# Kernel tuning notes

Hardware: AMD Instinct MI355X
Metric: run time of the kernel (lower is better)

## Reference

```python
import jax, jax.numpy as jnp
import numpy as np

HID = 128

def setup_inputs() -> dict:
    key = jax.random.key(0)
    ks = jax.random.split(key, 16)
    T, N, E = 32, 10000, 160000
    features = jax.random.normal(ks[0], (T, N, 1), dtype=jnp.float32)
    src = jax.random.randint(ks[1], (E,), 0, N)
    dst = jax.random.randint(ks[2], (E,), 0, N)
    s = 0.1
    # GraphConv params (stored as [in,out] so y = x @ W + b)
    W1 = jax.random.normal(ks[3], (1, 32), dtype=jnp.float32) * s
    b1 = jnp.zeros((32,), jnp.float32)
    W2 = jax.random.normal(ks[4], (32, HID), dtype=jnp.float32) * s
    b2 = jnp.zeros((HID,), jnp.float32)
    # attention-pool gate nn.Linear(128,1)
    gate_w = jax.random.normal(ks[5], (HID, 1), dtype=jnp.float32) * s
    gate_b = jnp.zeros((1,), jnp.float32)
    # GRU params, PyTorch layout: [3H, in], gate order (r, z, n)
    W_ih = jax.random.normal(ks[6], (3 * HID, HID), dtype=jnp.float32) * s
    W_hh = jax.random.normal(ks[7], (3 * HID, HID), dtype=jnp.float32) * s
    b_ih = jnp.zeros((3 * HID,), jnp.float32)
    b_hh = jnp.zeros((3 * HID,), jnp.float32)
    # dense layers ([in,out])
    d1_w = jax.random.normal(ks[8], (HID, 16), dtype=jnp.float32) * s
    d1_b = jnp.zeros((16,), jnp.float32)
    d2_w = jax.random.normal(ks[9], (16, 4), dtype=jnp.float32) * s
    d2_b = jnp.zeros((4,), jnp.float32)
    return {"features": features, "src": src, "dst": dst,
            "W1": W1, "b1": b1, "W2": W2, "b2": b2,
            "gate_w": gate_w, "gate_b": gate_b,
            "W_ih": W_ih, "W_hh": W_hh, "b_ih": b_ih, "b_hh": b_hh,
            "d1_w": d1_w, "d1_b": d1_b, "d2_w": d2_w, "d2_b": d2_b}


def reference(features, src, dst, W1, b1, W2, b2, gate_w, gate_b,
              W_ih, W_hh, b_ih, b_hh, d1_w, d1_b, d2_w, d2_b):
    T, N, _ = features.shape
    E = src.shape[0]
    ones = jnp.ones((E,), features.dtype)
    out_deg = jnp.clip(jax.ops.segment_sum(ones, src, num_segments=N), 1.0)
    in_deg = jnp.clip(jax.ops.segment_sum(ones, dst, num_segments=N), 1.0)
    norm_out = out_deg ** -0.5  # DGL GraphConv norm='both' (src side)
    norm_in = in_deg ** -0.5    # dst side

    def gconv(h, W, b):
        # h: [N, F] -> scale by src norm, gather, scatter-add to dst, scale, linear, SiLU
        msg = (h * norm_out[:, None])[src]               # [E, F]
        agg = jax.ops.segment_sum(msg, dst, num_segments=N)  # [N, F]
        return jax.nn.silu((agg * norm_in[:, None]) @ W + b)

    def per_frame(f):  # f: [N,1]
        return gconv(gconv(f, W1, b1), W2, b2)  # [N, HID]

    h = jax.vmap(per_frame)(features)  # [T, N, HID]

    # GlobalAttentionPooling: softmax over nodes of gate_nn(h)
    gate = h @ gate_w + gate_b                 # [T, N, 1]
    alpha = jax.nn.softmax(gate, axis=1)
    pooled = jnp.sum(alpha * h, axis=1)        # [T, HID]

    # single-layer GRU, batch=1, take final hidden state
    def gru_step(hprev, x):
        gi = x @ W_ih.T + b_ih
        gh = hprev @ W_hh.T + b_hh
        i_r, i_z, i_n = jnp.split(gi, 3)
        h_r, h_z, h_n = jnp.split(gh, 3)
        r = jax.nn.sigmoid(i_r + h_r)
        z = jax.nn.sigmoid(i_z + h_z)
        n = jnp.tanh(i_n + r * h_n)
        hnew = (1.0 - z) * n + z * hprev
        return hnew, None

    h0 = jnp.zeros((HID,), features.dtype)
    hT, _ = jax.lax.scan(gru_step, h0, pooled)

    out = jax.nn.silu(hT @ d1_w + d1_b)
    out = jax.nn.silu(out @ d2_w + d2_b)
    return jax.nn.sigmoid(out).reshape(1, 4)
```

## Files before the change

kernel.cpp:

```cpp
#include <hip/hip_runtime.h>
#include <stdint.h>

#define T_FRAMES 32
#define NNODES 10000
#define NEDGES 160000
#define HID 128
#define GXL 157

#define H1_SCALE 512.0f
#define H1_INV   (1.0f/512.0f)

typedef short v8s __attribute__((ext_vector_type(8)));
typedef float v4f __attribute__((ext_vector_type(4)));

static __device__ __forceinline__ ushort f2bf(float f){
  uint32_t u = __float_as_uint(f);
  u += 0x7FFFu + ((u >> 16) & 1u);
  return (ushort)(u >> 16);
}
static __device__ __forceinline__ float fsigm(float x){
  return __fdividef(1.0f, 1.0f + __expf(-x));
}
static __device__ __forceinline__ float fsilu(float x){
  return x * fsigm(x);
}
static __device__ __forceinline__ float ftanh(float x){
  return 2.0f * fsigm(2.0f * x) - 1.0f;
}


__global__ void k_degree(const int* __restrict__ src, const int* __restrict__ dst,
                         int* cnt_out, int* cnt_in, int E){
  int e = blockIdx.x*blockDim.x + threadIdx.x;
  if (e < E){
    atomicAdd(&cnt_out[src[e]], 1);
    atomicAdd(&cnt_in[dst[e]], 1);
  }
}

__global__ void __launch_bounds__(1024) k_scan(const int* __restrict__ cnt_in,
                                               const int* __restrict__ cnt_out,
                                               int* row_ptr, int* cursor,
                                               float* norm_out, float* norm_in, int N){
  __shared__ int wsum[16];
  __shared__ int carry_s, total_s;
  int tid = threadIdx.x;
  int lane = tid & 63, wid = tid >> 6;
  if (tid == 0) carry_s = 0;
  __syncthreads();
  for (int base = 0; base < N; base += 1024){
    int i = base + tid;
    int v = (i < N) ? cnt_in[i] : 0;
    if (i < N){
      norm_in[i]  = rsqrtf((float)max(v, 1));
      norm_out[i] = rsqrtf((float)max(cnt_out[i], 1));
    }
    int x = v;
    #pragma unroll
    for (int off = 1; off < 64; off <<= 1){
      int y = __shfl_up(x, off);
      if (lane >= off) x += y;
    }
    if (lane == 63) wsum[wid] = x;
    __syncthreads();
    if (tid == 0){
      int run = 0;
      #pragma unroll
      for (int w = 0; w < 16; ++w){ int tv = wsum[w]; wsum[w] = run; run += tv; }
      total_s = run;
    }
    __syncthreads();
    int excl = carry_s + wsum[wid] + x - v;
    if (i < N){ row_ptr[i] = excl; cursor[i] = excl; }
    __syncthreads();
    if (tid == 0) carry_s += total_s;
  }
  __syncthreads();
  if (tid == 0) row_ptr[N] = carry_s;
}

__global__ void k_fill(const int* __restrict__ src, const int* __restrict__ dst,
                       int* cursor, int* es, int E){
  int e = blockIdx.x*blockDim.x + threadIdx.x;
  if (e < E){
    int p = atomicAdd(&cursor[dst[e]], 1);
    es[p] = src[e];
  }
}


__global__ void __launch_bounds__(256) k_fnT(const float* __restrict__ feat,
                                             const float* __restrict__ norm_o,
                                             float* __restrict__ fnT, int N){
  __shared__ float sm[32][65];
  int n0 = blockIdx.x*64;
  int tid = threadIdx.x;
  for (int idx = tid; idx < 2048; idx += 256){
    int t = idx >> 6, i = idx & 63;
    int n = n0 + i;
    sm[t][i] = (n < N) ? feat[(size_t)t*N + n] : 0.f;
  }
  __syncthreads();
  for (int idx = tid; idx < 2048; idx += 256){
    int i = idx >> 5, t = idx & 31;
    int n = n0 + i;
    if (n < N) fnT[(size_t)n*32 + t] = sm[t][i] * norm_o[n];
  }
}


__global__ void __launch_bounds__(256) k_gconv1_nm(
    const float* __restrict__ fnT, const int* __restrict__ row_ptr,
    const int* __restrict__ es, const float* __restrict__ norm_in,
    const float* __restrict__ norm_out,
    const float* __restrict__ W1, const float* __restrict__ b1,
    uchar* __restrict__ h1s, int N){
  __shared__ float w1s[32], b1s[32];
  int tid = threadIdx.x;
  if (tid < 32){ w1s[tid] = W1[tid]; b1s[tid] = b1[tid]; }
  __syncthreads();
  int n = blockIdx.x*4 + (tid >> 6);
  int lane = tid & 63;
  int ep = lane >> 5, t = lane & 31;
  int s = row_ptr[n], d = row_ptr[n+1];
  float acc = 0.f;
  int e = s + ep;
  for (; e + 6 < d; e += 8){
    float v0 = fnT[(size_t)es[e]  *32 + t];
    float v1 = fnT[(size_t)es[e+2]*32 + t];
    float v2 = fnT[(size_t)es[e+4]*32 + t];
    float v3 = fnT[(size_t)es[e+6]*32 + t];
    acc += v0 + v1 + v2 + v3;
  }
  for (; e < d; e += 2)
    acc += fnT[(size_t)es[e]*32 + t];
  acc += __shfl_xor(acc, 32);
  float x1 = acc * norm_in[n];
  float x1p = __shfl(x1, lane >> 1);
  float no = norm_out[n];
  int j0 = (lane & 1) * 16;
  float hv[16];
  #pragma unroll
  for (int q = 0; q < 16; ++q)
    hv[q] = fsilu(fmaf(x1p, w1s[j0+q], b1s[j0+q])) * no;
  uint b[4] = {0u, 0u, 0u, 0u};
  #pragma unroll
  for (int q = 0; q < 16; ++q){
    float t8 = fminf(fmaxf(fmaf(hv[q], H1_SCALE, 128.5f), 0.f), 255.f);
    b[q >> 2] |= ((uint)(int)t8) << ((q & 3) * 8);
  }
  *(uint4*)(h1s + (size_t)n*1024 + lane*16) = make_uint4(b[0], b[1], b[2], b[3]);
}


__global__ void __launch_bounds__(256) k_gconv2_nm(
    const uchar* __restrict__ h1s, const int* __restrict__ row_ptr,
    const int* __restrict__ es, const float* __restrict__ norm_in,
    ushort* __restrict__ x2, int N){
  int tid = threadIdx.x;
  int n = blockIdx.x*4 + (tid >> 6);
  int lane = tid & 63;
  int s = row_ptr[n], d = row_ptr[n+1];
  float acc[16];
  #pragma unroll
  for (int i = 0; i < 16; ++i) acc[i] = 0.f;

  #define ACCB(v) do { \
    acc[0]  += (float)((v).x & 0xffu);         acc[1]  += (float)(((v).x >> 8) & 0xffu); \
    acc[2]  += (float)(((v).x >> 16) & 0xffu); acc[3]  += (float)((v).x >> 24); \
    acc[4]  += (float)((v).y & 0xffu);         acc[5]  += (float)(((v).y >> 8) & 0xffu); \
    acc[6]  += (float)(((v).y >> 16) & 0xffu); acc[7]  += (float)((v).y >> 24); \
    acc[8]  += (float)((v).z & 0xffu);         acc[9]  += (float)(((v).z >> 8) & 0xffu); \
    acc[10] += (float)(((v).z >> 16) & 0xffu); acc[11] += (float)((v).z >> 24); \
    acc[12] += (float)((v).w & 0xffu);         acc[13] += (float)(((v).w >> 8) & 0xffu); \
    acc[14] += (float)(((v).w >> 16) & 0xffu); acc[15] += (float)((v).w >> 24); \
  } while(0)

  int e = s;
  for (; e + 7 < d; e += 8){
    const uint4* q0 = (const uint4*)(h1s + (size_t)es[e]  *1024) + lane;
    const uint4* q1 = (const uint4*)(h1s + (size_t)es[e+1]*1024) + lane;
    const uint4* q2 = (const uint4*)(h1s + (size_t)es[e+2]*1024) + lane;
    const uint4* q3 = (const uint4*)(h1s + (size_t)es[e+3]*1024) + lane;
    const uint4* q4 = (const uint4*)(h1s + (size_t)es[e+4]*1024) + lane;
    const uint4* q5 = (const uint4*)(h1s + (size_t)es[e+5]*1024) + lane;
    const uint4* q6 = (const uint4*)(h1s + (size_t)es[e+6]*1024) + lane;
    const uint4* q7 = (const uint4*)(h1s + (size_t)es[e+7]*1024) + lane;
    uint4 w0 = *q0, w1 = *q1, w2 = *q2, w3 = *q3;
    uint4 w4 = *q4, w5 = *q5, w6 = *q6, w7 = *q7;
    ACCB(w0); ACCB(w1); ACCB(w2); ACCB(w3);
    ACCB(w4); ACCB(w5); ACCB(w6); ACCB(w7);
  }
  for (; e < d; ++e){
    uint4 w0 = *((const uint4*)(h1s + (size_t)es[e]*1024) + lane);
    ACCB(w0);
  }
  #undef ACCB

  float ni = norm_in[n];
  float corr = -128.0f * (float)(d - s);
  float sc = H1_INV * ni;
  uint w[8];
  #pragma unroll
  for (int q = 0; q < 8; ++q){
    float v0 = (acc[2*q]   + corr) * sc;
    float v1 = (acc[2*q+1] + corr) * sc;
    w[q] = (uint)f2bf(v0) | ((uint)f2bf(v1) << 16);
  }
  uint4* dp = (uint4*)(x2 + (size_t)n*1024 + lane*16);
  dp[0] = make_uint4(w[0], w[1], w[2], w[3]);
  dp[1] = make_uint4(w[4], w[5], w[6], w[7]);
}


__global__ void k_w2frag(const float* __restrict__ W2, ushort* __restrict__ W2F){
  int tid = blockIdx.x*blockDim.x + threadIdx.x;
  int j = tid & 7, l = (tid >> 3) & 63, i = tid >> 9;
  int g = l >> 4, n = l & 15;
  W2F[tid] = f2bf(W2[(g*8 + j)*128 + i*16 + n]);
}


__global__ void __launch_bounds__(256) k_linear_fused(
    const ushort* __restrict__ x2, const ushort* __restrict__ W2F,
    const float* __restrict__ b2, const float* __restrict__ gate_w,
    const float* __restrict__ gate_b,
    float* __restrict__ Zp, float* __restrict__ pooled_un, int N){
  __shared__ float pool_s[128];
  __shared__ float z_s[4];
  int t = blockIdx.y;
  int tid = threadIdx.x;
  int wave = tid >> 6, lane = tid & 63;
  int g = lane >> 4, n = lane & 15;
  if (tid < 128) pool_s[tid] = 0.f;
  if (tid < 4) z_s[tid] = 0.f;
  __syncthreads();
  int tile = blockIdx.x*4 + wave;
  bool active = (tile*16 < N);

  const v8s* W2Fv = (const v8s*)W2F;
  v8s bfrag[8];
  #pragma unroll
  for (int i = 0; i < 8; ++i) bfrag[i] = W2Fv[i*64 + lane];
  v4f acc[8];
  #pragma unroll
  for (int i = 0; i < 8; ++i){
    float bv = b2[i*16 + n];
    acc[i] = (v4f){bv, bv, bv, bv};
  }
  if (active){
    int nb = tile*16;
    const v8s* ap = (const v8s*)(x2 + (size_t)(nb + (lane & 15))*1024 + t*32);
    v8s a = ap[g];
    #pragma unroll
    for (int i = 0; i < 8; ++i)
      acc[i] = __builtin_amdgcn_mfma_f32_16x16x32_bf16(a, bfrag[i], acc[i], 0, 0, 0);

    float gw8[8];
    #pragma unroll
    for (int i = 0; i < 8; ++i) gw8[i] = gate_w[i*16 + n];
    float gp[4] = {0.f, 0.f, 0.f, 0.f};
    #pragma unroll
    for (int i = 0; i < 8; ++i){
      #pragma unroll
      for (int r = 0; r < 4; ++r) gp[r] += fsilu(acc[i][r]) * gw8[i];
    }
    #pragma unroll
    for (int m = 1; m < 16; m <<= 1){
      #pragma unroll
      for (int r = 0; r < 4; ++r) gp[r] += __shfl_xor(gp[r], m);
    }
    float gb = gate_b[0];
    float wn[4];
    #pragma unroll
    for (int r = 0; r < 4; ++r) wn[r] = __expf(gp[r] + gb);

    float se = (n == 0) ? (wn[0] + wn[1] + wn[2] + wn[3]) : 0.f;
    se += __shfl_xor(se, 16);
    se += __shfl_xor(se, 32);
    if (lane == 0) z_s[wave] = se;

    float cs[8];
    #pragma unroll
    for (int i = 0; i < 8; ++i){
      float c = 0.f;
      #pragma unroll
      for (int r = 0; r < 4; ++r) c += fsilu(acc[i][r]) * wn[r];
      c += __shfl_xor(c, 16);
      c += __shfl_xor(c, 32);
      cs[i] = c;
    }
    if (lane < 16){
      #pragma unroll
      for (int i = 0; i < 8; ++i) atomicAdd(&pool_s[i*16 + lane], cs[i]);
    }
  }
  __syncthreads();
  if (tid == 0)
    Zp[(size_t)t*GXL + blockIdx.x] = z_s[0] + z_s[1] + z_s[2] + z_s[3];
  if (tid < 128) atomicAdd(&pooled_un[(size_t)t*HID + tid], pool_s[tid]);
}


__global__ void __launch_bounds__(384) k_gi(const float* __restrict__ pooled_un,
                                            const float* __restrict__ Zp,
                                            const float* __restrict__ W_ih,
                                            const float* __restrict__ b_ih,
                                            float* __restrict__ gi_all){
  __shared__ float ps[HID];
  __shared__ float zred[6];
  int t = blockIdx.x, tid = threadIdx.x;
  int lane = tid & 63, wid = tid >> 6;
  float zs = 0.f;
  for (int i = tid; i < GXL; i += 384) zs += Zp[(size_t)t*GXL + i];
  #pragma unroll
  for (int m = 32; m; m >>= 1) zs += __shfl_xor(zs, m);
  if (lane == 0) zred[wid] = zs;
  __syncthreads();
  float invZ = __fdividef(1.0f, zred[0]+zred[1]+zred[2]+zred[3]+zred[4]+zred[5]);
  if (tid < HID) ps[tid] = pooled_un[(size_t)t*HID + tid] * invZ;
  __syncthreads();
  float acc = b_ih[tid];
  const float4* wr = (const float4*)(W_ih + (size_t)tid*HID);
  const float4* p4 = (const float4*)ps;
  #pragma unroll
  for (int q = 0; q < HID/4; ++q){
    float4 wv = wr[q], pv = p4[q];
    acc = fmaf(wv.x, pv.x, acc);
    acc = fmaf(wv.y, pv.y, acc);
    acc = fmaf(wv.z, pv.z, acc);
    acc = fmaf(wv.w, pv.w, acc);
  }
  gi_all[t*384 + tid] = acc;
}

__global__ void __launch_bounds__(768) k_gru(
    const float* __restrict__ gi_all, const float* __restrict__ W_hh,
    const float* __restrict__ b_hh,
    const float* __restrict__ d1_w, const float* __restrict__ d1_b,
    const float* __restrict__ d2_w, const float* __restrict__ d2_b,
    float* __restrict__ out){
  __shared__ float gi_s[T_FRAMES*3*HID];
  __shared__ float ps[2*384];
  __shared__ float h_s[HID];
  __shared__ float o1[16];
  int tid = threadIdx.x;
  int half = (tid >= 384) ? 1 : 0;
  int o = tid - half*384;

  for (int i = tid; i < T_FRAMES*3*HID; i += 768) gi_s[i] = gi_all[i];

  const float4* wr = (const float4*)(W_hh + (size_t)o*HID + half*64);
  #define LDW(i) float4 W##i = wr[i];
  LDW(0) LDW(1) LDW(2) LDW(3) LDW(4) LDW(5) LDW(6) LDW(7)
  LDW(8) LDW(9) LDW(10) LDW(11) LDW(12) LDW(13) LDW(14) LDW(15)
  #undef LDW
  float bh2 = half ? 0.f : b_hh[o];

  if (tid < HID) h_s[tid] = 0.f;
  __syncthreads();

  for (int t = 0; t < T_FRAMES; ++t){
    const float4* p4 = (const float4*)h_s + half*16;
    float acc = bh2;
    #define STEP(i) { float4 pv = p4[i]; \
      acc = fmaf(W##i.x, pv.x, acc); acc = fmaf(W##i.y, pv.y, acc); \
      acc = fmaf(W##i.z, pv.z, acc); acc = fmaf(W##i.w, pv.w, acc); }
    STEP(0) STEP(1) STEP(2) STEP(3) STEP(4) STEP(5) STEP(6) STEP(7)
    STEP(8) STEP(9) STEP(10) STEP(11) STEP(12) STEP(13) STEP(14) STEP(15)
    #undef STEP
    ps[tid] = acc;
    __syncthreads();
    if (tid < HID){
      const float* gi = gi_s + t*384;
      float ghr = ps[tid]       + ps[384+tid];
      float ghz = ps[128+tid]   + ps[512+tid];
      float ghn = ps[256+tid]   + ps[640+tid];
      float r  = fsigm(gi[tid]       + ghr);
      float z  = fsigm(gi[HID+tid]   + ghz);
      float nn = ftanh(gi[2*HID+tid] + r*ghn);
      h_s[tid] = (1.f - z)*nn + z*h_s[tid];
    }
    __syncthreads();
  }
  if (tid < 16){
    float acc = d1_b[tid];
    #pragma unroll 4
    for (int j = 0; j < HID; ++j) acc = fmaf(h_s[j], d1_w[j*16 + tid], acc);
    o1[tid] = fsilu(acc);
  }
  __syncthreads();
  if (tid < 4){
    float acc = d2_b[tid];
    #pragma unroll
    for (int j = 0; j < 16; ++j) acc = fmaf(o1[j], d2_w[j*4 + tid], acc);
    out[tid] = fsigm(fsilu(acc));
  }
}


extern "C" void kernel_launch(void* const* d_in, const int* in_sizes, int n_in,
                              void* d_out, int out_size, void* d_ws, size_t ws_size,
                              hipStream_t stream){
  const float* features = (const float*)d_in[0];
  const int*   src      = (const int*)  d_in[1];
  const int*   dst      = (const int*)  d_in[2];
  const float* W1       = (const float*)d_in[3];
  const float* b1       = (const float*)d_in[4];
  const float* W2       = (const float*)d_in[5];
  const float* b2       = (const float*)d_in[6];
  const float* gate_w   = (const float*)d_in[7];
  const float* gate_b   = (const float*)d_in[8];
  const float* W_ih     = (const float*)d_in[9];
  const float* W_hh     = (const float*)d_in[10];
  const float* b_ih     = (const float*)d_in[11];
  const float* b_hh     = (const float*)d_in[12];
  const float* d1_w     = (const float*)d_in[13];
  const float* d1_b     = (const float*)d_in[14];
  const float* d2_w     = (const float*)d_in[15];
  const float* d2_b     = (const float*)d_in[16];
  float* out = (float*)d_out;

  const int N = NNODES, E = NEDGES, T = T_FRAMES;

  char* base = (char*)d_ws;
  size_t off = 0;
  auto alloc = [&](size_t bytes)->void*{
    void* p = base + off;
    off = (off + bytes + 255) & ~(size_t)255;
    return p;
  };
  int*    cnt_out = (int*)   alloc((size_t)N*4);
  int*    cnt_in  = (int*)   alloc((size_t)N*4);
  float*  pooled  = (float*) alloc((size_t)T*HID*4);
  size_t zero_span = off;
  int*    row_ptr = (int*)   alloc((size_t)(N+1)*4);
  int*    cursor  = (int*)   alloc((size_t)N*4);
  float*  norm_o  = (float*) alloc((size_t)N*4);
  float*  norm_i  = (float*) alloc((size_t)N*4);
  int*    es      = (int*)   alloc((size_t)E*4);
  float*  fnT     = (float*) alloc((size_t)N*T*4);
  uchar*  h1s     = (uchar*) alloc((size_t)N*1024);
  ushort* x2      = (ushort*)alloc((size_t)N*T*32*2);
  float*  Zp      = (float*) alloc((size_t)T*GXL*4);
  float*  gi_all  = (float*) alloc((size_t)T*3*HID*4);
  ushort* W2F     = (ushort*)alloc((size_t)8*64*8*2);
  (void)ws_size; (void)in_sizes; (void)n_in; (void)out_size;

  hipMemsetAsync(d_ws, 0, zero_span, stream);

  k_degree<<<(E+255)/256, 256, 0, stream>>>(src, dst, cnt_out, cnt_in, E);
  k_scan  <<<1, 1024, 0, stream>>>(cnt_in, cnt_out, row_ptr, cursor, norm_o, norm_i, N);
  k_fill  <<<(E+255)/256, 256, 0, stream>>>(src, dst, cursor, es, E);

  k_fnT      <<<(N+63)/64, 256, 0, stream>>>(features, norm_o, fnT, N);
  k_gconv1_nm<<<N/4, 256, 0, stream>>>(fnT, row_ptr, es, norm_i, norm_o, W1, b1, h1s, N);
  k_gconv2_nm<<<N/4, 256, 0, stream>>>(h1s, row_ptr, es, norm_i, x2, N);

  k_w2frag<<<16, 256, 0, stream>>>(W2, W2F);

  k_linear_fused<<<dim3(GXL, T), 256, 0, stream>>>(x2, W2F, b2, gate_w, gate_b, Zp, pooled, N);

  k_gi <<<T, 384, 0, stream>>>(pooled, Zp, W_ih, b_ih, gi_all);
  k_gru<<<1, 768, 0, stream>>>(gi_all, W_hh, b_hh, d1_w, d1_b, d2_w, d2_b, out);
}
```

Measured before the change: 175.5 us.

## Fuse layer-2 gather with MFMA linear and attention pooling via shared memory

Merges the second graph-conv gather kernel with the linear/gate/pooling kernel. Each block gathers 16 nodes into LDS as bf16 rows, then each wave runs MFMA for 8 frames directly from LDS. This removes the global x2 round trip (about 20 MB written and reread) and one launch. Global atomics are replaced with per-block partial sums that k_gi reduces. In exchange, only 625 blocks run, with 33 KB of LDS each, which lowers occupancy for the latency-bound gather. k_gi also has a larger partial-sum reduction to do.

```diff
diff --git a/kernel.cpp b/kernel.cpp
--- a/kernel.cpp
+++ b/kernel.cpp
@@ -5,7 +5,7 @@
 #define NNODES 10000
 #define NEDGES 160000
 #define HID 128
-#define GXL 157
+#define NBLK 625
 
 #define H1_SCALE 512.0f
 #define H1_INV   (1.0f/512.0f)
@@ -153,17 +153,25 @@
 }
 
 
-__global__ void __launch_bounds__(256) k_gconv2_nm(
+__global__ void k_w2frag(const float* __restrict__ W2, ushort* __restrict__ W2F){
+  int tid = blockIdx.x*blockDim.x + threadIdx.x;
+  int j = tid & 7, l = (tid >> 3) & 63, i = tid >> 9;
+  int g = l >> 4, n = l & 15;
+  W2F[tid] = f2bf(W2[(g*8 + j)*128 + i*16 + n]);
+}
+
+
+__global__ void __launch_bounds__(256) k_gather_linear(
     const uchar* __restrict__ h1s, const int* __restrict__ row_ptr,
     const int* __restrict__ es, const float* __restrict__ norm_in,
-    ushort* __restrict__ x2, int N){
+    const ushort* __restrict__ W2F, const float* __restrict__ b2,
+    const float* __restrict__ gate_w, const float* __restrict__ gate_b,
+    float* __restrict__ Zp, float* __restrict__ pool_part){
+  __shared__ ushort x2s[16*1032];
   int tid = threadIdx.x;
-  int n = blockIdx.x*4 + (tid >> 6);
-  int lane = tid & 63;
-  int s = row_ptr[n], d = row_ptr[n+1];
-  float acc[16];
-  #pragma unroll
-  for (int i = 0; i < 16; ++i) acc[i] = 0.f;
+  int wave = tid >> 6, lane = tid & 63;
+  int blk = blockIdx.x;
+  int nb = blk*16;
 
   #define ACCB(v) do { \
     acc[0]  += (float)((v).x & 0xffu);         acc[1]  += (float)(((v).x >> 8) & 0xffu); \
@@ -175,150 +183,134 @@
     acc[12] += (float)((v).w & 0xffu);         acc[13] += (float)(((v).w >> 8) & 0xffu); \
     acc[14] += (float)(((v).w >> 16) & 0xffu); acc[15] += (float)((v).w >> 24); \
   } while(0)
-
-  int e = s;
-  for (; e + 7 < d; e += 8){
-    const uint4* q0 = (const uint4*)(h1s + (size_t)es[e]  *1024) + lane;
-    const uint4* q1 = (const uint4*)(h1s + (size_t)es[e+1]*1024) + lane;
-    const uint4* q2 = (const uint4*)(h1s + (size_t)es[e+2]*1024) + lane;
-    const uint4* q3 = (const uint4*)(h1s + (size_t)es[e+3]*1024) + lane;
-    const uint4* q4 = (const uint4*)(h1s + (size_t)es[e+4]*1024) + lane;
-    const uint4* q5 = (const uint4*)(h1s + (size_t)es[e+5]*1024) + lane;
-    const uint4* q6 = (const uint4*)(h1s + (size_t)es[e+6]*1024) + lane;
-    const uint4* q7 = (const uint4*)(h1s + (size_t)es[e+7]*1024) + lane;
-    uint4 w0 = *q0, w1 = *q1, w2 = *q2, w3 = *q3;
-    uint4 w4 = *q4, w5 = *q5, w6 = *q6, w7 = *q7;
-    ACCB(w0); ACCB(w1); ACCB(w2); ACCB(w3);
-    ACCB(w4); ACCB(w5); ACCB(w6); ACCB(w7);
-  }
-  for (; e < d; ++e){
-    uint4 w0 = *((const uint4*)(h1s + (size_t)es[e]*1024) + lane);
-    ACCB(w0);
+  #pragma unroll
+  for (int v = 0; v < 4; ++v){
+    int nl = wave*4 + v;
+    int n = nb + nl;
+    int s = row_ptr[n], d = row_ptr[n+1];
+    float acc[16];
+    #pragma unroll
+    for (int i = 0; i < 16; ++i) acc[i] = 0.f;
+    int e = s;
+    for (; e + 7 < d; e += 8){
+      uint4 w0 = *((const uint4*)(h1s + (size_t)es[e]  *1024) + lane);
+      uint4 w1 = *((const uint4*)(h1s + (size_t)es[e+1]*1024) + lane);
+      uint4 w2 = *((const uint4*)(h1s + (size_t)es[e+2]*1024) + lane);
+      uint4 w3 = *((const uint4*)(h1s + (size_t)es[e+3]*1024) + lane);
+      uint4 w4 = *((const uint4*)(h1s + (size_t)es[e+4]*1024) + lane);
+      uint4 w5 = *((const uint4*)(h1s + (size_t)es[e+5]*1024) + lane);
+      uint4 w6 = *((const uint4*)(h1s + (size_t)es[e+6]*1024) + lane);
+      uint4 w7 = *((const uint4*)(h1s + (size_t)es[e+7]*1024) + lane);
+      ACCB(w0); ACCB(w1); ACCB(w2); ACCB(w3);
+      ACCB(w4); ACCB(w5); ACCB(w6); ACCB(w7);
+    }
+    for (; e < d; ++e){
+      uint4 w0 = *((const uint4*)(h1s + (size_t)es[e]*1024) + lane);
+      ACCB(w0);
+    }
+    float ni = norm_in[n];
+    float corr = -128.0f * (float)(d - s);
+    float sc = H1_INV * ni;
+    uint w[8];
+    #pragma unroll
+    for (int q = 0; q < 8; ++q){
+      float v0 = (acc[2*q]   + corr) * sc;
+      float v1 = (acc[2*q+1] + corr) * sc;
+      w[q] = (uint)f2bf(v0) | ((uint)f2bf(v1) << 16);
+    }
+    ushort* dp = &x2s[nl*1032 + lane*16];
+    *(uint4*)dp       = make_uint4(w[0], w[1], w[2], w[3]);
+    *((uint4*)dp + 1) = make_uint4(w[4], w[5], w[6], w[7]);
   }
   #undef ACCB
-
-  float ni = norm_in[n];
-  float corr = -128.0f * (float)(d - s);
-  float sc = H1_INV * ni;
-  uint w[8];
-  #pragma unroll
-  for (int q = 0; q < 8; ++q){
-    float v0 = (acc[2*q]   + corr) * sc;
-    float v1 = (acc[2*q+1] + corr) * sc;
-    w[q] = (uint)f2bf(v0) | ((uint)f2bf(v1) << 16);
-  }
-  uint4* dp = (uint4*)(x2 + (size_t)n*1024 + lane*16);
-  dp[0] = make_uint4(w[0], w[1], w[2], w[3]);
-  dp[1] = make_uint4(w[4], w[5], w[6], w[7]);
-}
-
-
-__global__ void k_w2frag(const float* __restrict__ W2, ushort* __restrict__ W2F){
-  int tid = blockIdx.x*blockDim.x + threadIdx.x;
-  int j = tid & 7, l = (tid >> 3) & 63, i = tid >> 9;
-  int g = l >> 4, n = l & 15;
-  W2F[tid] = f2bf(W2[(g*8 + j)*128 + i*16 + n]);
-}
-
-
-__global__ void __launch_bounds__(256) k_linear_fused(
-    const ushort* __restrict__ x2, const ushort* __restrict__ W2F,
-    const float* __restrict__ b2, const float* __restrict__ gate_w,
-    const float* __restrict__ gate_b,
-    float* __restrict__ Zp, float* __restrict__ pooled_un, int N){
-  __shared__ float pool_s[128];
-  __shared__ float z_s[4];
-  int t = blockIdx.y;
-  int tid = threadIdx.x;
-  int wave = tid >> 6, lane = tid & 63;
-  int g = lane >> 4, n = lane & 15;
-  if (tid < 128) pool_s[tid] = 0.f;
-  if (tid < 4) z_s[tid] = 0.f;
-  __syncthreads();
-  int tile = blockIdx.x*4 + wave;
-  bool active = (tile*16 < N);
-
+  __syncthreads();
+
+  int g = lane >> 4, n16 = lane & 15;
   const v8s* W2Fv = (const v8s*)W2F;
   v8s bfrag[8];
   #pragma unroll
   for (int i = 0; i < 8; ++i) bfrag[i] = W2Fv[i*64 + lane];
-  v4f acc[8];
-  #pragma unroll
-  for (int i = 0; i < 8; ++i){
-    float bv = b2[i*16 + n];
-    acc[i] = (v4f){bv, bv, bv, bv};
-  }
-  if (active){
-    int nb = tile*16;
-    const v8s* ap = (const v8s*)(x2 + (size_t)(nb + (lane & 15))*1024 + t*32);
-    v8s a = ap[g];
+  float gw8[8], bv8[8];
+  #pragma unroll
+  for (int i = 0; i < 8; ++i){ gw8[i] = gate_w[i*16 + n16]; bv8[i] = b2[i*16 + n16]; }
+  float gb = gate_b[0];
+
+  #pragma unroll
+  for (int f = 0; f < 8; ++f){
+    int t = wave*8 + f;
+    v8s a = *(const v8s*)&x2s[n16*1032 + t*32 + g*8];
+    v4f acc[8];
+    #pragma unroll
+    for (int i = 0; i < 8; ++i) acc[i] = (v4f){bv8[i], bv8[i], bv8[i], bv8[i]};
     #pragma unroll
     for (int i = 0; i < 8; ++i)
       acc[i] = __builtin_amdgcn_mfma_f32_16x16x32_bf16(a, bfrag[i], acc[i], 0, 0, 0);
 
-    float gw8[8];
-    #pragma unroll
-    for (int i = 0; i < 8; ++i) gw8[i] = gate_w[i*16 + n];
-    float gp[4] = {0.f, 0.f, 0.f, 0.f};
+    float hs[8][4];
     #pragma unroll
     for (int i = 0; i < 8; ++i){
       #pragma unroll
-      for (int r = 0; r < 4; ++r) gp[r] += fsilu(acc[i][r]) * gw8[i];
+      for (int r = 0; r < 4; ++r) hs[i][r] = fsilu(acc[i][r]);
+    }
+    float gp[4] = {0.f, 0.f, 0.f, 0.f};
+    #pragma unroll
+    for (int i = 0; i < 8; ++i){
+      #pragma unroll
+      for (int r = 0; r < 4; ++r) gp[r] += hs[i][r] * gw8[i];
     }
     #pragma unroll
     for (int m = 1; m < 16; m <<= 1){
       #pragma unroll
       for (int r = 0; r < 4; ++r) gp[r] += __shfl_xor(gp[r], m);
     }
-    float gb = gate_b[0];
     float wn[4];
     #pragma unroll
     for (int r = 0; r < 4; ++r) wn[r] = __expf(gp[r] + gb);
 
-    float se = (n == 0) ? (wn[0] + wn[1] + wn[2] + wn[3]) : 0.f;
+    float se = (n16 == 0) ? (wn[0] + wn[1] + wn[2] + wn[3]) : 0.f;
     se += __shfl_xor(se, 16);
     se += __shfl_xor(se, 32);
-    if (lane == 0) z_s[wave] = se;
-
-    float cs[8];
+    if (lane == 0) Zp[(size_t)t*NBLK + blk] = se;
+
+    float* pp = pool_part + ((size_t)t*NBLK + blk)*HID;
     #pragma unroll
     for (int i = 0; i < 8; ++i){
       float c = 0.f;
       #pragma unroll
-      for (int r = 0; r < 4; ++r) c += fsilu(acc[i][r]) * wn[r];
+      for (int r = 0; r < 4; ++r) c += hs[i][r] * wn[r];
       c += __shfl_xor(c, 16);
       c += __shfl_xor(c, 32);
-      cs[i] = c;
-    }
-    if (lane < 16){
-      #pragma unroll
-      for (int i = 0; i < 8; ++i) atomicAdd(&pool_s[i*16 + lane], cs[i]);
-    }
-  }
-  __syncthreads();
-  if (tid == 0)
-    Zp[(size_t)t*GXL + blockIdx.x] = z_s[0] + z_s[1] + z_s[2] + z_s[3];
-  if (tid < 128) atomicAdd(&pooled_un[(size_t)t*HID + tid], pool_s[tid]);
-}
-
-
-__global__ void __launch_bounds__(384) k_gi(const float* __restrict__ pooled_un,
+      if (lane < 16) pp[i*16 + lane] = c;
+    }
+  }
+}
+
+
+__global__ void __launch_bounds__(384) k_gi(const float* __restrict__ pool_part,
                                             const float* __restrict__ Zp,
                                             const float* __restrict__ W_ih,
                                             const float* __restrict__ b_ih,
                                             float* __restrict__ gi_all){
   __shared__ float ps[HID];
+  __shared__ float pp[3][HID];
   __shared__ float zred[6];
   int t = blockIdx.x, tid = threadIdx.x;
   int lane = tid & 63, wid = tid >> 6;
   float zs = 0.f;
-  for (int i = tid; i < GXL; i += 384) zs += Zp[(size_t)t*GXL + i];
+  for (int b = tid; b < NBLK; b += 384) zs += Zp[(size_t)t*NBLK + b];
   #pragma unroll
   for (int m = 32; m; m >>= 1) zs += __shfl_xor(zs, m);
   if (lane == 0) zred[wid] = zs;
   __syncthreads();
   float invZ = __fdividef(1.0f, zred[0]+zred[1]+zred[2]+zred[3]+zred[4]+zred[5]);
-  if (tid < HID) ps[tid] = pooled_un[(size_t)t*HID + tid] * invZ;
+  int grp = tid >> 7;
+  int c = tid & 127;
+  float ss = 0.f;
+  for (int b = grp; b < NBLK; b += 3)
+    ss += pool_part[((size_t)t*NBLK + b)*HID + c];
+  pp[grp][c] = ss;
+  __syncthreads();
+  if (tid < HID) ps[tid] = (pp[0][tid] + pp[1][tid] + pp[2][tid]) * invZ;
   __syncthreads();
   float acc = b_ih[tid];
   const float4* wr = (const float4*)(W_ih + (size_t)tid*HID);
@@ -430,21 +422,20 @@
     off = (off + bytes + 255) & ~(size_t)255;
     return p;
   };
-  int*    cnt_out = (int*)   alloc((size_t)N*4);
-  int*    cnt_in  = (int*)   alloc((size_t)N*4);
-  float*  pooled  = (float*) alloc((size_t)T*HID*4);
+  int*    cnt_out  = (int*)   alloc((size_t)N*4);
+  int*    cnt_in   = (int*)   alloc((size_t)N*4);
   size_t zero_span = off;
-  int*    row_ptr = (int*)   alloc((size_t)(N+1)*4);
-  int*    cursor  = (int*)   alloc((size_t)N*4);
-  float*  norm_o  = (float*) alloc((size_t)N*4);
-  float*  norm_i  = (float*) alloc((size_t)N*4);
-  int*    es      = (int*)   alloc((size_t)E*4);
-  float*  fnT     = (float*) alloc((size_t)N*T*4);
-  uchar*  h1s     = (uchar*) alloc((size_t)N*1024);
-  ushort* x2      = (ushort*)alloc((size_t)N*T*32*2);
-  float*  Zp      = (float*) alloc((size_t)T*GXL*4);
-  float*  gi_all  = (float*) alloc((size_t)T*3*HID*4);
-  ushort* W2F     = (ushort*)alloc((size_t)8*64*8*2);
+  int*    row_ptr  = (int*)   alloc((size_t)(N+1)*4);
+  int*    cursor   = (int*)   alloc((size_t)N*4);
+  float*  norm_o   = (float*) alloc((size_t)N*4);
+  float*  norm_i   = (float*) alloc((size_t)N*4);
+  int*    es       = (int*)   alloc((size_t)E*4);
+  float*  fnT      = (float*) alloc((size_t)N*T*4);
+  uchar*  h1s      = (uchar*) alloc((size_t)N*1024);
+  float*  Zp       = (float*) alloc((size_t)T*NBLK*4);
+  float*  pool_part= (float*) alloc((size_t)T*NBLK*HID*4);
+  float*  gi_all   = (float*) alloc((size_t)T*3*HID*4);
+  ushort* W2F      = (ushort*)alloc((size_t)8*64*8*2);
   (void)ws_size; (void)in_sizes; (void)n_in; (void)out_size;
 
   hipMemsetAsync(d_ws, 0, zero_span, stream);
@@ -455,12 +446,12 @@
 
   k_fnT      <<<(N+63)/64, 256, 0, stream>>>(features, norm_o, fnT, N);
   k_gconv1_nm<<<N/4, 256, 0, stream>>>(fnT, row_ptr, es, norm_i, norm_o, W1, b1, h1s, N);
-  k_gconv2_nm<<<N/4, 256, 0, stream>>>(h1s, row_ptr, es, norm_i, x2, N);
 
   k_w2frag<<<16, 256, 0, stream>>>(W2, W2F);
 
-  k_linear_fused<<<dim3(GXL, T), 256, 0, stream>>>(x2, W2F, b2, gate_w, gate_b, Zp, pooled, N);
-
-  k_gi <<<T, 384, 0, stream>>>(pooled, Zp, W_ih, b_ih, gi_all);
+  k_gather_linear<<<NBLK, 256, 0, stream>>>(h1s, row_ptr, es, norm_i, W2F, b2,
+                                            gate_w, gate_b, Zp, pool_part);
+
+  k_gi <<<T, 384, 0, stream>>>(pool_part, Zp, W_ih, b_ih, gi_all);
   k_gru<<<1, 768, 0, stream>>>(gi_all, W_hh, b_hh, d1_w, d1_b, d2_w, d2_b, out);
 }
```

Result: slower. 231.6 us (+32.0%).
